# Performance work log

Measured on AMD Instinct MI355X. Metric: run time of the kernel, lower is better.

The kernel has to match this reference:

```python
import jax, jax.numpy as jnp
import numpy as np

B, C, L = 4, 64, 4096
RED = 4          # reduction -> q/k channels = C // RED = 16
N_HASHES = 4
HASH_BUCKETS = min(L // 4, 32)  # = 32, matches torch code
EPS = 1e-5


def _conv1x1(x, W, b):
    # x: [B, Cin, L], W: [Cout, Cin], b: [Cout]
    return jnp.einsum('bcl,oc->bol', x, W) + b[None, :, None]


def setup_inputs() -> dict:
    key = jax.random.key(0)
    ks = jax.random.split(key, 12)
    Cq = C // RED
    x = jax.random.normal(ks[0], (B, C, L), dtype=jnp.float32)
    hash_idx = jax.random.randint(ks[1], (B, N_HASHES, L), 0, HASH_BUCKETS, dtype=jnp.int32)
    sC = 1.0 / np.sqrt(C)
    Wq = jax.random.normal(ks[2], (Cq, C), dtype=jnp.float32) * sC
    bq = jax.random.normal(ks[3], (Cq,), dtype=jnp.float32) * 0.01
    Wk = jax.random.normal(ks[4], (Cq, C), dtype=jnp.float32) * sC
    bk = jax.random.normal(ks[5], (Cq,), dtype=jnp.float32) * 0.01
    Wv = jax.random.normal(ks[6], (C, C), dtype=jnp.float32) * sC
    bv = jax.random.normal(ks[7], (C,), dtype=jnp.float32) * 0.01
    Wo = jax.random.normal(ks[8], (C, C), dtype=jnp.float32) * sC
    bo = jax.random.normal(ks[9], (C,), dtype=jnp.float32) * 0.01
    gamma = jax.random.normal(ks[10], (1,), dtype=jnp.float32)  # nonzero so attn path matters
    bn_w = jnp.ones((C,), dtype=jnp.float32)
    bn_b = jnp.zeros((C,), dtype=jnp.float32)
    return dict(x=x, hash_idx=hash_idx, Wq=Wq, bq=bq, Wk=Wk, bk=bk,
                Wv=Wv, bv=bv, Wo=Wo, bo=bo, gamma=gamma, bn_w=bn_w, bn_b=bn_b)


def reference(x, hash_idx, Wq, bq, Wk, bk, Wv, bv, Wo, bo, gamma, bn_w, bn_b):
    # 1x1 conv projections
    q = _conv1x1(x, Wq, bq)   # [B, C/RED, L]
    k = _conv1x1(x, Wk, bk)   # [B, C/RED, L]
    v = _conv1x1(x, Wv, bv)   # [B, C, L]

    qT = q.transpose(0, 2, 1)  # [B, L, Cq]
    kT = k.transpose(0, 2, 1)
    vT = v.transpose(0, 2, 1)  # [B, L, C]

    # raw scores are hash-independent; only the bucket mask changes per hash
    scores = jnp.einsum('bic,bjc->bij', qT, kT)  # [B, L, L], no sqrt(d) scaling (matches torch)

    n_hashes = hash_idx.shape[1]
    acc = jnp.zeros_like(vT)
    for h in range(n_hashes):  # small fixed loop
        idx = hash_idx[:, h, :]                       # [B, L]
        mask = idx[:, :, None] == idx[:, None, :]     # same-bucket mask [B, L, L]
        s = jnp.where(mask, scores, -1e9)
        attn = jax.nn.softmax(s, axis=-1)             # within-bucket softmax (diag always valid)
        acc = acc + jnp.einsum('bij,bjc->bic', attn, vT)
    attn_out = (acc / n_hashes).transpose(0, 2, 1)    # [B, C, L], averaged over hashes

    out = _conv1x1(attn_out, Wo, bo)
    out = gamma * out + x                             # residual with learned scalar

    # BatchNorm1d, training mode: biased batch stats over (B, L) per channel
    mean = out.mean(axis=(0, 2), keepdims=True)
    var = out.var(axis=(0, 2), keepdims=True)
    out = (out - mean) * jax.lax.rsqrt(var + EPS)
    out = out * bn_w[None, :, None] + bn_b[None, :, None]
    return out
```

## Files before the change

kernel.cpp:

```cpp
#include <hip/hip_runtime.h>
#include <math.h>

#define Bn 4
#define Cn 64
#define Ln 4096
#define CQ 16
#define NH 4
#define NB 32
#define EPSV 1e-5f

#define MAXS 384
#define SFULL 192

#define QSZ   (Bn*Ln*CQ)
#define VSZ   (Bn*Ln*Cn)
#define ACCSZ (Bn*Ln*Cn)
#define NBH   (Bn*NH)

#define OFF_K   QSZ
#define OFF_V   (2*QSZ)
#define OFF_ACC (2*QSZ + VSZ)

#define LOG2E 1.44269504088896f
#define WSTR 36
#define XSTR 65
#define OSTR 68
#define NBLK_O 512

__global__ __launch_bounds__(512) void proj_kernel(
        const float* __restrict__ x,
        const float* __restrict__ Wq, const float* __restrict__ bq,
        const float* __restrict__ Wk, const float* __restrict__ bk,
        const float* __restrict__ Wv, const float* __restrict__ bv,
        float* __restrict__ q, float* __restrict__ k, float* __restrict__ v) {
    __shared__ float sWt[Cn*WSTR];
    __shared__ float sX[Cn*XSTR];
    __shared__ float sb[32];
    int tid = threadIdx.x;
    int third = blockIdx.x % 3;
    int pg    = blockIdx.x / 3;
    int rbase = third * 32;
    {
        int rr = tid >> 4, c4 = (tid & 15) * 4;
        int r = rbase + rr;
        float4 w;
        if (r < 16)      w = *(const float4*)&Wq[r*Cn + c4];
        else if (r < 32) w = *(const float4*)&Wk[(r-16)*Cn + c4];
        else             w = *(const float4*)&Wv[(r-32)*Cn + c4];
        sWt[(c4+0)*WSTR + rr] = w.x;
        sWt[(c4+1)*WSTR + rr] = w.y;
        sWt[(c4+2)*WSTR + rr] = w.z;
        sWt[(c4+3)*WSTR + rr] = w.w;
    }
    if (tid < 32) {
        int r = rbase + tid;
        sb[tid] = (r < 16) ? bq[r] : (r < 32 ? bk[r-16] : bv[r-32]);
    }
    int gp0 = pg * 64;
    int b = gp0 >> 12, l0 = gp0 & (Ln - 1);
    const float* xb = &x[(size_t)b*Cn*Ln + l0];
    #pragma unroll
    for (int r2 = 0; r2 < 2; r2++) {
        int j = r2*512 + tid;
        int c = j >> 4, l4 = (j & 15) * 4;
        float4 t = *(const float4*)&xb[c*Ln + l4];
        sX[c*XSTR + l4+0] = t.x;
        sX[c*XSTR + l4+1] = t.y;
        sX[c*XSTR + l4+2] = t.z;
        sX[c*XSTR + l4+3] = t.w;
    }
    __syncthreads();
    int p = tid & 63, og = tid >> 6;
    int gp = gp0 + p;
    int rr0 = og * 4;
    float val[4];
    #pragma unroll
    for (int i = 0; i < 4; i++) val[i] = sb[rr0 + i];
    #pragma unroll
    for (int c = 0; c < Cn; c++) {
        float xv = sX[c*XSTR + p];
        const float4 wa = *(const float4*)&sWt[c*WSTR + rr0];
        val[0] = fmaf(wa.x, xv, val[0]); val[1] = fmaf(wa.y, xv, val[1]);
        val[2] = fmaf(wa.z, xv, val[2]); val[3] = fmaf(wa.w, xv, val[3]);
    }
    float4 t0 = make_float4(val[0], val[1], val[2], val[3]);
    float4* q4 = (float4*)&q[gp*CQ];
    float4* k4 = (float4*)&k[gp*CQ];
    float4* v4 = (float4*)&v[gp*Cn];
    if (third == 0)      { if (og < 4) q4[og] = t0; else k4[og-4] = t0; }
    else if (third == 1) { v4[og]   = t0; }
    else                 { v4[og+8] = t0; }
}

__device__ __forceinline__ float quad_reduce_sum(float d) {
    d += __int_as_float(__builtin_amdgcn_mov_dpp(__float_as_int(d), 0xB1, 0xF, 0xF, true));
    d += __int_as_float(__builtin_amdgcn_mov_dpp(__float_as_int(d), 0x4E, 0xF, 0xF, true));
    return d;
}

__device__ __forceinline__ float rowsum16(float x) {
    x += __int_as_float(__builtin_amdgcn_mov_dpp(__float_as_int(x), 0x114, 0xF, 0xF, true));
    x += __int_as_float(__builtin_amdgcn_mov_dpp(__float_as_int(x), 0x118, 0xF, 0xF, true));
    return x;
}

template<int NS> struct Sweep {
    float4 qr[NS];
    float4 o[NS][4];
    float  lsum[NS];
    int    ir[NS];
};

template<int NS>
__device__ __forceinline__ void sweep_init(Sweep<NS>& st, int q0, int S, int act,
        const int* list, const float4* Q4, int qq, int c4) {
    #pragma unroll
    for (int s = 0; s < NS; s++) {
        int qi = q0 + s*4 + qq;
        int a = act && (qi < S);
        st.ir[s] = a ? list[qi] : -1;
        float4 t = make_float4(0.f, 0.f, 0.f, 0.f);
        if (a) {
            t = Q4[(size_t)st.ir[s]*4 + c4];
            t.x *= LOG2E; t.y *= LOG2E; t.z *= LOG2E; t.w *= LOG2E;
        }
        st.qr[s] = t;
        st.lsum[s] = 0.f;
        #pragma unroll
        for (int tt = 0; tt < 4; tt++) st.o[s][tt] = make_float4(0.f, 0.f, 0.f, 0.f);
    }
}

template<int NS, bool MASKED>
__device__ __forceinline__ void kb_step(Sweep<NS>& st, int kb, int nkv,
        const float4* ks4, const float4* vs4, int l15, int kk,
        int i0, int i1, int i2, int i3) {
    const float4 kq = ks4[kb*16 + l15];
    const float4 va = vs4[kb*64 + i0*16 + l15];
    const float4 vb = vs4[kb*64 + i1*16 + l15];
    const float4 vc = vs4[kb*64 + i2*16 + l15];
    const float4 vd = vs4[kb*64 + i3*16 + l15];
    #pragma unroll
    for (int s = 0; s < NS; s++) {
        float d = st.qr[s].x * kq.x;
        d = fmaf(st.qr[s].y, kq.y, d);
        d = fmaf(st.qr[s].z, kq.z, d);
        d = fmaf(st.qr[s].w, kq.w, d);
        d = quad_reduce_sum(d);
        float pw = __builtin_amdgcn_exp2f(d);
        if (MASKED) pw = ((kb*4 + kk) < nkv) ? pw : 0.f;
        st.lsum[s] += pw;
        st.o[s][0].x = fmaf(pw, va.x, st.o[s][0].x); st.o[s][0].y = fmaf(pw, va.y, st.o[s][0].y);
        st.o[s][0].z = fmaf(pw, va.z, st.o[s][0].z); st.o[s][0].w = fmaf(pw, va.w, st.o[s][0].w);
        st.o[s][1].x = fmaf(pw, vb.x, st.o[s][1].x); st.o[s][1].y = fmaf(pw, vb.y, st.o[s][1].y);
        st.o[s][1].z = fmaf(pw, vb.z, st.o[s][1].z); st.o[s][1].w = fmaf(pw, vb.w, st.o[s][1].w);
        st.o[s][2].x = fmaf(pw, vc.x, st.o[s][2].x); st.o[s][2].y = fmaf(pw, vc.y, st.o[s][2].y);
        st.o[s][2].z = fmaf(pw, vc.z, st.o[s][2].z); st.o[s][2].w = fmaf(pw, vc.w, st.o[s][2].w);
        st.o[s][3].x = fmaf(pw, vd.x, st.o[s][3].x); st.o[s][3].y = fmaf(pw, vd.y, st.o[s][3].y);
        st.o[s][3].z = fmaf(pw, vd.z, st.o[s][3].z); st.o[s][3].w = fmaf(pw, vd.w, st.o[s][3].w);
    }
}

template<int NS>
__device__ __forceinline__ void sweep_keys(Sweep<NS>& st, int nk,
        const float4* ks4, const float4* vs4, int l15, int kk,
        int i0, int i1, int i2, int i3) {
    int nf = nk >> 2;
    for (int kb = 0; kb < nf; kb++)
        kb_step<NS,false>(st, kb, nk, ks4, vs4, l15, kk, i0, i1, i2, i3);
    if (nk & 3)
        kb_step<NS,true>(st, nf, nk, ks4, vs4, l15, kk, i0, i1, i2, i3);
}

template<int NS, int MODE>
__device__ __forceinline__ void sweep_fin(Sweep<NS>& st, float* __restrict__ acc,
        int b, int h, int qq, int lane, int c4) {
    #pragma unroll
    for (int s = 0; s < NS; s++) {
        st.lsum[s] = rowsum16(st.lsum[s]);
        #pragma unroll
        for (int t = 0; t < 4; t++) {
            st.o[s][t].x = rowsum16(st.o[s][t].x);
            st.o[s][t].y = rowsum16(st.o[s][t].y);
            st.o[s][t].z = rowsum16(st.o[s][t].z);
            st.o[s][t].w = rowsum16(st.o[s][t].w);
        }
    }
    if ((lane & 15) < 12) return;
    #pragma unroll
    for (int s = 0; s < NS; s++) {
        if (st.ir[s] >= 0) {
            float inv = 1.f / st.lsum[s];
            #pragma unroll
            for (int t = 0; t < 4; t++) {
                float4 r;
                r.x = st.o[s][t].x * inv; r.y = st.o[s][t].y * inv;
                r.z = st.o[s][t].z * inv; r.w = st.o[s][t].w * inv;
                int ch = ((qq + t) & 3)*16 + c4*4;
                if (MODE == 1) {
                    *(float4*)&acc[(((size_t)h*Bn + b)*Ln + st.ir[s])*Cn + ch] = r;
                } else {
                    float* ap = &acc[((size_t)b*Ln + st.ir[s])*Cn + ch];
                    atomicAdd(&ap[0], r.x); atomicAdd(&ap[1], r.y);
                    atomicAdd(&ap[2], r.z); atomicAdd(&ap[3], r.w);
                }
            }
        }
    }
}

template<int NS, int MODE>
__device__ __forceinline__ void run_sweep(int q0, int S, int act,
        const int* list, const float4* Q4,
        const float4* ks4, const float4* vs4, float* __restrict__ acc,
        int b, int h, int qq, int lane, int c4, int l15, int kk,
        int i0, int i1, int i2, int i3) {
    Sweep<NS> st;
    sweep_init<NS>(st, q0, S, act, list, Q4, qq, c4);
    sweep_keys<NS>(st, S, ks4, vs4, l15, kk, i0, i1, i2, i3);
    sweep_fin<NS,MODE>(st, acc, b, h, qq, lane, c4);
}

__device__ __forceinline__ void stage_kv(int tid, int nk, int k0, const int* list,
        const float4* K4, const float4* V4, float4* ks4, float4* vs4) {
    const float4 z = make_float4(0.f, 0.f, 0.f, 0.f);
    int nb4 = (nk + 3) >> 2;
    for (int G = tid; G < nb4*16; G += 512) {
        int j = G >> 2;
        ks4[G] = (j < nk) ? K4[(size_t)list[k0 + j]*4 + (G & 3)] : z;
    }
    for (int F = tid; F < nb4*64; F += 512) {
        int kb = F >> 6, ii = (F >> 4) & 3, k2 = (F >> 2) & 3, cc = F & 3;
        int j = kb*4 + k2;
        vs4[F] = (j < nk) ? V4[(size_t)list[k0 + j]*16 + ii*4 + cc] : z;
    }
}

template<int MODE>
__global__ __launch_bounds__(512, 2) void attn_kernel(
        const float* __restrict__ q, const float* __restrict__ k,
        const float* __restrict__ v, const int* __restrict__ hidx,
        float* __restrict__ acc) {
    __shared__ int list[MAXS];
    __shared__ int wtot[8];
    __shared__ float4 ks4[SFULL*4];
    __shared__ float4 vs4[SFULL*16];
    int blk = blockIdx.x;
    int u  = blk & (NB-1);
    int bh = blk >> 5;
    int b  = bh >> 2;
    int h  = bh & 3;
    int tid = threadIdx.x;

    const int4* hp4 = (const int4*)&hidx[bh*Ln + tid*8];
    int hv[8];
    #pragma unroll
    for (int t = 0; t < 2; t++) {
        int4 tmp = hp4[t];
        hv[t*4+0]=tmp.x; hv[t*4+1]=tmp.y; hv[t*4+2]=tmp.z; hv[t*4+3]=tmp.w;
    }
    int myCnt = 0;
    #pragma unroll
    for (int t = 0; t < 8; t++) myCnt += (hv[t] == u);
    int lane = tid & 63, wv = tid >> 6;
    int pre = myCnt;
    #pragma unroll
    for (int d = 1; d < 64; d <<= 1) {
        int t = __shfl_up(pre, d, 64);
        if (lane >= d) pre += t;
    }
    if (lane == 63) wtot[wv] = pre;
    __syncthreads();
    int base = 0, Sall = 0;
    #pragma unroll
    for (int w = 0; w < 8; w++) {
        base += (w < wv) ? wtot[w] : 0;
        Sall += wtot[w];
    }
    int S = min(Sall, MAXS);
    int excl = base + pre - myCnt;
    #pragma unroll
    for (int t = 0; t < 8; t++) {
        if (hv[t] == u) {
            if (excl < MAXS) list[excl] = tid*8 + t;
            excl++;
        }
    }
    __syncthreads();

    int qq = (lane >> 4) & 3;
    int kk = (lane >> 2) & 3;
    int c4 = lane & 3;
    int l15 = lane & 15;
    int i0 = qq, i1 = (qq+1)&3, i2 = (qq+2)&3, i3 = (qq+3)&3;
    const float4* Q4 = (const float4*)&q[(size_t)b*Ln*CQ];
    const float4* K4 = (const float4*)&k[(size_t)b*Ln*CQ];
    const float4* V4 = (const float4*)&v[(size_t)b*Ln*Cn];

    if (S <= SFULL) {
        stage_kv(tid, S, 0, list, K4, V4, ks4, vs4);
        __syncthreads();
        if (wv*16 < S)
            run_sweep<4,MODE>(wv*16, S, 1, list, Q4, ks4, vs4, acc,
                              b, h, qq, lane, c4, l15, kk, i0, i1, i2, i3);
        for (int qb = 128 + wv*4; qb < S; qb += 32)
            run_sweep<1,MODE>(qb, S, 1, list, Q4, ks4, vs4, acc,
                              b, h, qq, lane, c4, l15, kk, i0, i1, i2, i3);
    } else {
        for (int q0s = 0; q0s < S; q0s += 128) {
            int q0 = q0s + wv*16;
            int act = q0 < S;
            Sweep<4> st;
            sweep_init<4>(st, q0, S, act, list, Q4, qq, c4);
            for (int k0 = 0; k0 < S; k0 += SFULL) {
                int nk = min(SFULL, S - k0);
                __syncthreads();
                stage_kv(tid, nk, k0, list, K4, V4, ks4, vs4);
                __syncthreads();
                if (act) sweep_keys<4>(st, nk, ks4, vs4, l15, kk, i0, i1, i2, i3);
            }
            if (act) sweep_fin<4,MODE>(st, acc, b, h, qq, lane, c4);
        }
    }
}

template<int MODE>
__global__ __launch_bounds__(256) void outconv_kernel(
        const float* __restrict__ acc, const float* __restrict__ Wo,
        const float* __restrict__ bo, const float* __restrict__ gamma,
        const float* __restrict__ x, float* __restrict__ y,
        float* __restrict__ Psum, float* __restrict__ Psq) {
    __shared__ float sWt[Cn*OSTR];
    __shared__ float sA[Cn*33];
    __shared__ float sb[Cn];
    int tid = threadIdx.x;
    int pg = blockIdx.x;
    for (int idx = tid; idx < Cn*Cn; idx += 256) {
        int c = idx & 63, o = idx >> 6;
        sWt[c*OSTR + o] = Wo[o*Cn + c];
    }
    if (tid < Cn) sb[tid] = bo[tid];
    const float4* a4 = (const float4*)&acc[(size_t)pg*32*Cn];
    #pragma unroll
    for (int r = 0; r < 2; r++) {
        int idx = r*256 + tid;
        int p = idx >> 4, c0 = (idx & 15) * 4;
        float4 t = a4[idx];
        if (MODE == 1) {
            float4 t1 = a4[(size_t)ACCSZ/4   + idx];
            float4 t2 = a4[(size_t)ACCSZ/4*2 + idx];
            float4 t3 = a4[(size_t)ACCSZ/4*3 + idx];
            t.x += t1.x + t2.x + t3.x; t.y += t1.y + t2.y + t3.y;
            t.z += t1.z + t2.z + t3.z; t.w += t1.w + t2.w + t3.w;
        }
        sA[(c0+0)*33 + p] = t.x*0.25f;
        sA[(c0+1)*33 + p] = t.y*0.25f;
        sA[(c0+2)*33 + p] = t.z*0.25f;
        sA[(c0+3)*33 + p] = t.w*0.25f;
    }
    __syncthreads();
    float g = gamma[0];
    int p = tid & 31, og = tid >> 5;
    int gp = pg * 32 + p;
    int b = gp >> 12, l = gp & (Ln - 1);
    int o0 = og * 8;
    float val[8];
    #pragma unroll
    for (int i = 0; i < 8; i++) val[i] = sb[o0 + i];
    #pragma unroll
    for (int c = 0; c < Cn; c++) {
        float av = sA[c*33 + p];
        const float4 wa = *(const float4*)&sWt[c*OSTR + o0];
        const float4 wb = *(const float4*)&sWt[c*OSTR + o0 + 4];
        val[0] = fmaf(wa.x, av, val[0]); val[1] = fmaf(wa.y, av, val[1]);
        val[2] = fmaf(wa.z, av, val[2]); val[3] = fmaf(wa.w, av, val[3]);
        val[4] = fmaf(wb.x, av, val[4]); val[5] = fmaf(wb.y, av, val[5]);
        val[6] = fmaf(wb.z, av, val[6]); val[7] = fmaf(wb.w, av, val[7]);
    }
    float yv8[8];
    #pragma unroll
    for (int i = 0; i < 8; i++) {
        int o = o0 + i;
        float yv = fmaf(g, val[i], x[((size_t)b*Cn + o)*Ln + l]);
        y[((size_t)b*Cn + o)*Ln + l] = yv;
        yv8[i] = yv;
    }
    __syncthreads();
    #pragma unroll
    for (int i = 0; i < 8; i++) sA[(o0+i)*33 + p] = yv8[i];
    __syncthreads();
    if (tid < Cn) {
        float s = 0.f, s2 = 0.f;
        #pragma unroll 4
        for (int pp = 0; pp < 32; pp++) {
            float yv = sA[tid*33 + pp];
            s += yv;
            s2 = fmaf(yv, yv, s2);
        }
        Psum[tid*NBLK_O + pg] = s;
        Psq [tid*NBLK_O + pg] = s2;
    }
}

__global__ __launch_bounds__(256) void norm_kernel(
        const float* __restrict__ y,
        const float* __restrict__ Psum, const float* __restrict__ Psq,
        const float* __restrict__ bnw, const float* __restrict__ bnb,
        float* __restrict__ out) {
    int tid = threadIdx.x;
    int c = (blockIdx.x >> 2) & 63;
    float s  = Psum[c*NBLK_O + tid] + Psum[c*NBLK_O + 256 + tid];
    float s2 = Psq [c*NBLK_O + tid] + Psq [c*NBLK_O + 256 + tid];
    #pragma unroll
    for (int w = 1; w < 64; w <<= 1) {
        s  += __shfl_xor(s,  w, 64);
        s2 += __shfl_xor(s2, w, 64);
    }
    __shared__ float rs[4], rs2[4];
    int wv = tid >> 6;
    if ((tid & 63) == 0) { rs[wv] = s; rs2[wv] = s2; }
    __syncthreads();
    s  = (rs[0]+rs[1]) + (rs[2]+rs[3]);
    s2 = (rs2[0]+rs2[1]) + (rs2[2]+rs2[3]);
    const float n = (float)(Bn*Ln);
    float mu = s / n;
    float var = s2 / n - mu*mu;
    float is = rsqrtf(var + EPSV);
    float w = is * bnw[c];
    float bb = bnb[c] - mu * w;
    int idx = blockIdx.x * 256 + tid;
    float4 t = ((const float4*)y)[idx];
    float4 r;
    r.x = t.x*w + bb; r.y = t.y*w + bb; r.z = t.z*w + bb; r.w = t.w*w + bb;
    ((float4*)out)[idx] = r;
}

extern "C" void kernel_launch(void* const* d_in, const int* in_sizes, int n_in,
                              void* d_out, int out_size, void* d_ws, size_t ws_size,
                              hipStream_t stream) {
    const float* x    = (const float*)d_in[0];
    const int*   hidx = (const int*)  d_in[1];
    const float* Wq   = (const float*)d_in[2];
    const float* bq   = (const float*)d_in[3];
    const float* Wk   = (const float*)d_in[4];
    const float* bk   = (const float*)d_in[5];
    const float* Wv   = (const float*)d_in[6];
    const float* bv   = (const float*)d_in[7];
    const float* Wo   = (const float*)d_in[8];
    const float* bo   = (const float*)d_in[9];
    const float* gam  = (const float*)d_in[10];
    const float* bnw  = (const float*)d_in[11];
    const float* bnb  = (const float*)d_in[12];
    float* out = (float*)d_out;

    float* ws  = (float*)d_ws;
    float* q   = ws;
    float* k   = ws + OFF_K;
    float* v   = ws + OFF_V;
    float* acc = ws + OFF_ACC;
    float* y   = ws;

    const size_t bigNeed = ((size_t)OFF_ACC + 4*(size_t)ACCSZ
                            + 2*(size_t)Cn*NBLK_O) * sizeof(float);
    bool big = ws_size >= bigNeed;
    size_t accN = big ? 4*(size_t)ACCSZ : (size_t)ACCSZ;
    float* Psum = acc + accN;
    float* Psq  = Psum + (size_t)Cn*NBLK_O;

    proj_kernel<<<Bn*Ln/64*3, 512, 0, stream>>>(x, Wq, bq, Wk, bk, Wv, bv, q, k, v);
    if (big) {
        attn_kernel<1><<<NBH*NB, 512, 0, stream>>>(q, k, v, hidx, acc);
        outconv_kernel<1><<<NBLK_O, 256, 0, stream>>>(acc, Wo, bo, gam, x, y, Psum, Psq);
    } else {
        hipMemsetAsync(acc, 0, (size_t)ACCSZ*sizeof(float), stream);
        attn_kernel<0><<<NBH*NB, 512, 0, stream>>>(q, k, v, hidx, acc);
        outconv_kernel<0><<<NBLK_O, 256, 0, stream>>>(acc, Wo, bo, gam, x, y, Psum, Psq);
    }
    norm_kernel<<<Bn*Cn*Ln/4/256, 256, 0, stream>>>(y, Psum, Psq, bnw, bnb, out);
}
```

Measured before the change: 150.7 us.

## Drop LDS staging of K/V and split each bucket across two smaller blocks

The attention kernel no longer stages gathered K/V rows into shared memory. Each wave now reads K and V directly from global memory through the bucket index list, relying on the caches. Each bucket is split over two 256-thread blocks that divide the queries between them, and the launch bounds are raised so more blocks fit per CU. This removes the staging barriers and the separate path for large buckets, at the cost of redundant global gathers per wave and a duplicated bucket-list scan in each block.

New measurement: 343.0 us. 128% more time.

```diff
diff --git a/kernel.cpp b/kernel.cpp
--- a/kernel.cpp
+++ b/kernel.cpp
@@ -10,7 +10,6 @@
 #define EPSV 1e-5f
 
 #define MAXS 384
-#define SFULL 192
 
 #define QSZ   (Bn*Ln*CQ)
 #define VSZ   (Bn*Ln*Cn)
@@ -112,12 +111,12 @@
 };
 
 template<int NS>
-__device__ __forceinline__ void sweep_init(Sweep<NS>& st, int q0, int S, int act,
+__device__ __forceinline__ void sweep_init(Sweep<NS>& st, int q0, int S,
         const int* list, const float4* Q4, int qq, int c4) {
     #pragma unroll
     for (int s = 0; s < NS; s++) {
         int qi = q0 + s*4 + qq;
-        int a = act && (qi < S);
+        int a = (qi < S);
         st.ir[s] = a ? list[qi] : -1;
         float4 t = make_float4(0.f, 0.f, 0.f, 0.f);
         if (a) {
@@ -133,13 +132,17 @@
 
 template<int NS, bool MASKED>
 __device__ __forceinline__ void kb_step(Sweep<NS>& st, int kb, int nkv,
-        const float4* ks4, const float4* vs4, int l15, int kk,
-        int i0, int i1, int i2, int i3) {
-    const float4 kq = ks4[kb*16 + l15];
-    const float4 va = vs4[kb*64 + i0*16 + l15];
-    const float4 vb = vs4[kb*64 + i1*16 + l15];
-    const float4 vc = vs4[kb*64 + i2*16 + l15];
-    const float4 vd = vs4[kb*64 + i3*16 + l15];
+        const int* list, const float4* K4, const float4* V4,
+        int kk, int c4, int i0, int i1, int i2, int i3) {
+    int j = kb*4 + kk;
+    int jc = MASKED ? min(j, nkv - 1) : j;
+    int lv = list[jc];
+    const float4 kq = K4[(size_t)lv*4 + c4];
+    const float4* vb4 = &V4[(size_t)lv*16 + c4];
+    const float4 va = vb4[i0*4];
+    const float4 vb = vb4[i1*4];
+    const float4 vc = vb4[i2*4];
+    const float4 vd = vb4[i3*4];
     #pragma unroll
     for (int s = 0; s < NS; s++) {
         float d = st.qr[s].x * kq.x;
@@ -148,7 +151,7 @@
         d = fmaf(st.qr[s].w, kq.w, d);
         d = quad_reduce_sum(d);
         float pw = __builtin_amdgcn_exp2f(d);
-        if (MASKED) pw = ((kb*4 + kk) < nkv) ? pw : 0.f;
+        if (MASKED) pw = (j < nkv) ? pw : 0.f;
         st.lsum[s] += pw;
         st.o[s][0].x = fmaf(pw, va.x, st.o[s][0].x); st.o[s][0].y = fmaf(pw, va.y, st.o[s][0].y);
         st.o[s][0].z = fmaf(pw, va.z, st.o[s][0].z); st.o[s][0].w = fmaf(pw, va.w, st.o[s][0].w);
@@ -163,13 +166,13 @@
 
 template<int NS>
 __device__ __forceinline__ void sweep_keys(Sweep<NS>& st, int nk,
-        const float4* ks4, const float4* vs4, int l15, int kk,
-        int i0, int i1, int i2, int i3) {
+        const int* list, const float4* K4, const float4* V4,
+        int kk, int c4, int i0, int i1, int i2, int i3) {
     int nf = nk >> 2;
     for (int kb = 0; kb < nf; kb++)
-        kb_step<NS,false>(st, kb, nk, ks4, vs4, l15, kk, i0, i1, i2, i3);
+        kb_step<NS,false>(st, kb, nk, list, K4, V4, kk, c4, i0, i1, i2, i3);
     if (nk & 3)
-        kb_step<NS,true>(st, nf, nk, ks4, vs4, l15, kk, i0, i1, i2, i3);
+        kb_step<NS,true>(st, nf, nk, list, K4, V4, kk, c4, i0, i1, i2, i3);
 }
 
 template<int NS, int MODE>
@@ -210,58 +213,42 @@
 }
 
 template<int NS, int MODE>
-__device__ __forceinline__ void run_sweep(int q0, int S, int act,
-        const int* list, const float4* Q4,
-        const float4* ks4, const float4* vs4, float* __restrict__ acc,
-        int b, int h, int qq, int lane, int c4, int l15, int kk,
+__device__ __forceinline__ void run_sweep(int q0, int S,
+        const int* list, const float4* Q4, const float4* K4, const float4* V4,
+        float* __restrict__ acc,
+        int b, int h, int qq, int lane, int c4, int kk,
         int i0, int i1, int i2, int i3) {
     Sweep<NS> st;
-    sweep_init<NS>(st, q0, S, act, list, Q4, qq, c4);
-    sweep_keys<NS>(st, S, ks4, vs4, l15, kk, i0, i1, i2, i3);
+    sweep_init<NS>(st, q0, S, list, Q4, qq, c4);
+    sweep_keys<NS>(st, S, list, K4, V4, kk, c4, i0, i1, i2, i3);
     sweep_fin<NS,MODE>(st, acc, b, h, qq, lane, c4);
 }
 
-__device__ __forceinline__ void stage_kv(int tid, int nk, int k0, const int* list,
-        const float4* K4, const float4* V4, float4* ks4, float4* vs4) {
-    const float4 z = make_float4(0.f, 0.f, 0.f, 0.f);
-    int nb4 = (nk + 3) >> 2;
-    for (int G = tid; G < nb4*16; G += 512) {
-        int j = G >> 2;
-        ks4[G] = (j < nk) ? K4[(size_t)list[k0 + j]*4 + (G & 3)] : z;
-    }
-    for (int F = tid; F < nb4*64; F += 512) {
-        int kb = F >> 6, ii = (F >> 4) & 3, k2 = (F >> 2) & 3, cc = F & 3;
-        int j = kb*4 + k2;
-        vs4[F] = (j < nk) ? V4[(size_t)list[k0 + j]*16 + ii*4 + cc] : z;
-    }
-}
-
 template<int MODE>
-__global__ __launch_bounds__(512, 2) void attn_kernel(
+__global__ __launch_bounds__(256, 5) void attn_kernel(
         const float* __restrict__ q, const float* __restrict__ k,
         const float* __restrict__ v, const int* __restrict__ hidx,
         float* __restrict__ acc) {
     __shared__ int list[MAXS];
-    __shared__ int wtot[8];
-    __shared__ float4 ks4[SFULL*4];
-    __shared__ float4 vs4[SFULL*16];
+    __shared__ int wtot[4];
     int blk = blockIdx.x;
+    int qs = blk >> 9;
     int u  = blk & (NB-1);
-    int bh = blk >> 5;
+    int bh = (blk >> 5) & (NBH-1);
     int b  = bh >> 2;
     int h  = bh & 3;
     int tid = threadIdx.x;
 
-    const int4* hp4 = (const int4*)&hidx[bh*Ln + tid*8];
-    int hv[8];
-    #pragma unroll
-    for (int t = 0; t < 2; t++) {
+    const int4* hp4 = (const int4*)(&hidx[bh*Ln] + tid*16);
+    int hv[16];
+    #pragma unroll
+    for (int t = 0; t < 4; t++) {
         int4 tmp = hp4[t];
         hv[t*4+0]=tmp.x; hv[t*4+1]=tmp.y; hv[t*4+2]=tmp.z; hv[t*4+3]=tmp.w;
     }
     int myCnt = 0;
     #pragma unroll
-    for (int t = 0; t < 8; t++) myCnt += (hv[t] == u);
+    for (int t = 0; t < 16; t++) myCnt += (hv[t] == u);
     int lane = tid & 63, wv = tid >> 6;
     int pre = myCnt;
     #pragma unroll
@@ -273,16 +260,16 @@
     __syncthreads();
     int base = 0, Sall = 0;
     #pragma unroll
-    for (int w = 0; w < 8; w++) {
+    for (int w = 0; w < 4; w++) {
         base += (w < wv) ? wtot[w] : 0;
         Sall += wtot[w];
     }
     int S = min(Sall, MAXS);
     int excl = base + pre - myCnt;
     #pragma unroll
-    for (int t = 0; t < 8; t++) {
+    for (int t = 0; t < 16; t++) {
         if (hv[t] == u) {
-            if (excl < MAXS) list[excl] = tid*8 + t;
+            if (excl < MAXS) list[excl] = tid*16 + t;
             excl++;
         }
     }
@@ -291,37 +278,18 @@
     int qq = (lane >> 4) & 3;
     int kk = (lane >> 2) & 3;
     int c4 = lane & 3;
-    int l15 = lane & 15;
     int i0 = qq, i1 = (qq+1)&3, i2 = (qq+2)&3, i3 = (qq+3)&3;
     const float4* Q4 = (const float4*)&q[(size_t)b*Ln*CQ];
     const float4* K4 = (const float4*)&k[(size_t)b*Ln*CQ];
     const float4* V4 = (const float4*)&v[(size_t)b*Ln*Cn];
 
-    if (S <= SFULL) {
-        stage_kv(tid, S, 0, list, K4, V4, ks4, vs4);
-        __syncthreads();
-        if (wv*16 < S)
-            run_sweep<4,MODE>(wv*16, S, 1, list, Q4, ks4, vs4, acc,
-                              b, h, qq, lane, c4, l15, kk, i0, i1, i2, i3);
-        for (int qb = 128 + wv*4; qb < S; qb += 32)
-            run_sweep<1,MODE>(qb, S, 1, list, Q4, ks4, vs4, acc,
-                              b, h, qq, lane, c4, l15, kk, i0, i1, i2, i3);
-    } else {
-        for (int q0s = 0; q0s < S; q0s += 128) {
-            int q0 = q0s + wv*16;
-            int act = q0 < S;
-            Sweep<4> st;
-            sweep_init<4>(st, q0, S, act, list, Q4, qq, c4);
-            for (int k0 = 0; k0 < S; k0 += SFULL) {
-                int nk = min(SFULL, S - k0);
-                __syncthreads();
-                stage_kv(tid, nk, k0, list, K4, V4, ks4, vs4);
-                __syncthreads();
-                if (act) sweep_keys<4>(st, nk, ks4, vs4, l15, kk, i0, i1, i2, i3);
-            }
-            if (act) sweep_fin<4,MODE>(st, acc, b, h, qq, lane, c4);
-        }
-    }
+    int q0 = qs*64 + wv*16;
+    if (q0 < S)
+        run_sweep<4,MODE>(q0, S, list, Q4, K4, V4, acc,
+                          b, h, qq, lane, c4, kk, i0, i1, i2, i3);
+    for (int qb = 128 + (qs*4 + wv)*4; qb < S; qb += 32)
+        run_sweep<1,MODE>(qb, S, list, Q4, K4, V4, acc,
+                          b, h, qq, lane, c4, kk, i0, i1, i2, i3);
 }
 
 template<int MODE>
@@ -469,11 +437,11 @@
 
     proj_kernel<<<Bn*Ln/64*3, 512, 0, stream>>>(x, Wq, bq, Wk, bk, Wv, bv, q, k, v);
     if (big) {
-        attn_kernel<1><<<NBH*NB, 512, 0, stream>>>(q, k, v, hidx, acc);
+        attn_kernel<1><<<NBH*NB*2, 256, 0, stream>>>(q, k, v, hidx, acc);
         outconv_kernel<1><<<NBLK_O, 256, 0, stream>>>(acc, Wo, bo, gam, x, y, Psum, Psq);
     } else {
         hipMemsetAsync(acc, 0, (size_t)ACCSZ*sizeof(float), stream);
-        attn_kernel<0><<<NBH*NB, 512, 0, stream>>>(q, k, v, hidx, acc);
+        attn_kernel<0><<<NBH*NB*2, 256, 0, stream>>>(q, k, v, hidx, acc);
         outconv_kernel<0><<<NBLK_O, 256, 0, stream>>>(acc, Wo, bo, gam, x, y, Psum, Psq);
     }
     norm_kernel<<<Bn*Cn*Ln/4/256, 256, 0, stream>>>(y, Psum, Psq, bnw, bnb, out);
```
